# Kernel optimization log

Measured on AMD Instinct MI355X. Metric: run time of the kernel, lower is better.

Reference implementation:

```python
import jax, jax.numpy as jnp
import numpy as np

META_HIDDEN = 32


def _meta_apply(t, mw1, mb1, mw2, mb2):
    # t: [..., 3] triples; meta MLP 3 -> META_HIDDEN -> 1 (ReLU)
    h = jax.nn.relu(jnp.einsum('...k,hk->...h', t, mw1) + mb1)
    return jnp.einsum('...h,h->...', h, mw2[0]) + mb2[0]


def _meta_update_layer(v_in, w, v_out, mw1, mb1, mw2, mb2):
    # v_in: [I] (batch-0 input activations), w: [O, I], v_out: [O] (batch-0 output activations)
    # Builds the triples [v_i, w_ij, v_j] for every (i, j) pair and runs one batched meta pass.
    t = jnp.stack([
        jnp.broadcast_to(v_in[None, :], w.shape),
        w,
        jnp.broadcast_to(v_out[:, None], w.shape),
    ], axis=-1)  # [O, I, 3]
    return _meta_apply(t, mw1, mb1, mw2, mb2)  # [O, I] new weights


def setup_inputs() -> dict:
    key = jax.random.key(0)
    ks = jax.random.split(key, 12)
    I, H1, H2, O, B = 1024, 2048, 2048, 1024, 32
    def lin(kw, fan_in, fan_out):
        s = 1.0 / np.sqrt(fan_in)
        return jax.random.uniform(kw, (fan_out, fan_in), jnp.float32, -s, s)
    x = jax.random.normal(ks[0], (B, I), jnp.float32)
    w1 = lin(ks[1], I, H1); b1 = jax.random.uniform(ks[2], (H1,), jnp.float32, -1/np.sqrt(I), 1/np.sqrt(I))
    w2 = lin(ks[3], H1, H2); b2 = jax.random.uniform(ks[4], (H2,), jnp.float32, -1/np.sqrt(H1), 1/np.sqrt(H1))
    w3 = lin(ks[5], H2, O); b3 = jax.random.uniform(ks[6], (O,), jnp.float32, -1/np.sqrt(H2), 1/np.sqrt(H2))
    # meta network 3 -> META_HIDDEN -> 1
    mw1 = lin(ks[7], 3, META_HIDDEN); mb1 = jax.random.uniform(ks[8], (META_HIDDEN,), jnp.float32, -1/np.sqrt(3), 1/np.sqrt(3))
    mw2 = lin(ks[9], META_HIDDEN, 1); mb2 = jax.random.uniform(ks[10], (1,), jnp.float32, -1/np.sqrt(META_HIDDEN), 1/np.sqrt(META_HIDDEN))
    return {"x": x, "w1": w1, "b1": b1, "w2": w2, "b2": b2, "w3": w3, "b3": b3,
            "mw1": mw1, "mb1": mb1, "mw2": mw2, "mb2": mb2}


def reference(x, w1, b1, w2, b2, w3, b3, mw1, mb1, mw2, mb2):
    # Main 3-layer MLP forward (ReLU after every layer, including the last, as in the source).
    a0 = x
    a1 = jax.nn.relu(a0 @ w1.T + b1)
    a2 = jax.nn.relu(a1 @ w2.T + b2)
    out = jax.nn.relu(a2 @ w3.T + b3)
    # Per-weight meta update: original code loops over every (input, output) neuron pair of
    # each fc weight and writes meta_weight([v_i, w_ij, v_j]) back into the weight.
    # Only batch row 0 of the activations is used (impulse[i].data[0, idx]).
    nw1 = _meta_update_layer(a0[0], w1, a1[0], mw1, mb1, mw2, mb2)
    nw2 = _meta_update_layer(a1[0], w2, a2[0], mw1, mb1, mw2, mb2)
    nw3 = _meta_update_layer(a2[0], w3, out[0], mw1, mb1, mw2, mb2)
    return out, nw1, nw2, nw3
```

## Files before the change

kernel.cpp:

```cpp
#include <hip/hip_runtime.h>

#define NT 256

typedef unsigned int uint;
typedef unsigned short ushort_t;
typedef float f2 __attribute__((ext_vector_type(2)));
typedef short bh8 __attribute__((ext_vector_type(8)));
typedef float f32x4 __attribute__((ext_vector_type(4)));
typedef uint u32x4 __attribute__((ext_vector_type(4)));

__device__ __forceinline__ void gload16(const float* g, float* l) {
  __builtin_amdgcn_global_load_lds(
      (const __attribute__((address_space(1))) void*)g,
      (__attribute__((address_space(3))) void*)l, 16, 0, 0);
}

__device__ __forceinline__ uint hi2(float a, float b) {
  return (__float_as_uint(a) >> 16) | (__float_as_uint(b) & 0xffff0000u);
}
__device__ __forceinline__ uint lo2(float a, float b) {
  const float r0 = a - __uint_as_float(__float_as_uint(a) & 0xffff0000u);
  const float r1 = b - __uint_as_float(__float_as_uint(b) & 0xffff0000u);
  return hi2(r0, r1);
}
__device__ __forceinline__ void split8v(float4 v0, float4 v1, bh8& hi, bh8& lo) {
  u32x4 h = {hi2(v0.x, v0.y), hi2(v0.z, v0.w), hi2(v1.x, v1.y), hi2(v1.z, v1.w)};
  u32x4 t = {lo2(v0.x, v0.y), lo2(v0.z, v0.w), lo2(v1.x, v1.y), lo2(v1.z, v1.w)};
  hi = __builtin_bit_cast(bh8, h);
  lo = __builtin_bit_cast(bh8, t);
}

__device__ __forceinline__ void meta_body(
    int g,
    const float* __restrict__ w1, const float* __restrict__ w2, const float* __restrict__ w3,
    const float* __restrict__ a0, const float* __restrict__ r1, const float* __restrict__ r2,
    const float* __restrict__ bb1, const float* __restrict__ bb2, const float* __restrict__ bb3,
    float* __restrict__ n1, float* __restrict__ n2, float* __restrict__ n3,
    const float* __restrict__ mw1, const float* __restrict__ mb1,
    const float* __restrict__ mw2, const float* __restrict__ mb2) {
  const int n1c = (2048 * 1024) / 8;
  const int n2c = (2048 * 2048) / 8;

  const float* W; const float* vin; const float* bias; float* nw;
  int sh, e;
  if (g < n1c)            { W = w1; vin = a0; bias = bb1; nw = n1; sh = 10; e = g; }
  else if (g < n1c + n2c) { W = w2; vin = r1; bias = bb2; nw = n2; sh = 11; e = g - n1c; }
  else                    { W = w3; vin = r2; bias = bb3; nw = n3; sh = 11; e = g - n1c - n2c; }

  const int base = e << 3;
  const int o = base >> sh;
  const int i0 = base & ((1 << sh) - 1);
  const int tid = threadIdx.x;

  f2 wv[4], vv[4];
  {
    float4 t0 = *reinterpret_cast<const float4*>(&W[base]);
    float4 t1 = *reinterpret_cast<const float4*>(&W[base + 4]);
    wv[0] = (f2){t0.x, t0.y}; wv[1] = (f2){t0.z, t0.w};
    wv[2] = (f2){t1.x, t1.y}; wv[3] = (f2){t1.z, t1.w};
    float4 u0 = *reinterpret_cast<const float4*>(&vin[i0]);
    float4 u1 = *reinterpret_cast<const float4*>(&vin[i0 + 4]);
    vv[0] = (f2){u0.x, u0.y}; vv[1] = (f2){u0.z, u0.w};
    vv[2] = (f2){u1.x, u1.y}; vv[3] = (f2){u1.z, u1.w};
  }

  float part = 0.f;
  #pragma unroll
  for (int p = 0; p < 4; ++p)
    part += wv[p].x * vv[p].x + wv[p].y * vv[p].y;
  #pragma unroll
  for (int m = 32; m >= 1; m >>= 1)
    part += __shfl_xor(part, m, 64);
  __shared__ float msum[4];
  if ((tid & 63) == 0) msum[tid >> 6] = part;
  __syncthreads();
  float vo;
  if (sh == 10) vo = (tid < 128) ? (msum[0] + msum[1]) : (msum[2] + msum[3]);
  else          vo = (msum[0] + msum[1]) + (msum[2] + msum[3]);
  vo = fmaxf(vo + bias[o], 0.f);

  const float c2 = mb2[0];
  float r[32];
  #pragma unroll
  for (int j = 0; j < 32; ++j)
    r[j] = fmaf(mw1[3 * j + 2], vo, mb1[j]);

  f2 acc[4];
  #pragma unroll
  for (int p = 0; p < 4; ++p) acc[p] = (f2){c2, c2};

  const f2 zero = (f2){0.f, 0.f};
  #pragma unroll
  for (int j = 0; j < 32; ++j) {
    const float aj = mw1[3 * j];
    const float bj = mw1[3 * j + 1];
    const float mj = mw2[j];
    const f2 a2v = (f2){aj, aj};
    const f2 b2v = (f2){bj, bj};
    const f2 m2v = (f2){mj, mj};
    const f2 r2v = (f2){r[j], r[j]};
    #pragma unroll
    for (int p = 0; p < 4; ++p) {
#if __has_builtin(__builtin_elementwise_fma) && __has_builtin(__builtin_elementwise_max)
      f2 q = __builtin_elementwise_fma(a2v, vv[p], r2v);
      f2 h = __builtin_elementwise_fma(b2v, wv[p], q);
      h = __builtin_elementwise_max(h, zero);
      acc[p] = __builtin_elementwise_fma(m2v, h, acc[p]);
#else
      f2 h;
      h.x = fmaxf(fmaf(bj, wv[p].x, fmaf(aj, vv[p].x, r[j])), 0.f);
      h.y = fmaxf(fmaf(bj, wv[p].y, fmaf(aj, vv[p].y, r[j])), 0.f);
      acc[p].x = fmaf(mj, h.x, acc[p].x);
      acc[p].y = fmaf(mj, h.y, acc[p].y);
#endif
    }
  }

  *reinterpret_cast<float4*>(&nw[base])     = make_float4(acc[0].x, acc[0].y, acc[1].x, acc[1].y);
  *reinterpret_cast<float4*>(&nw[base + 4]) = make_float4(acc[2].x, acc[2].y, acc[3].x, acc[3].y);
}

template<int KL, int OBL, int AF32>
__device__ __forceinline__ void gemm_fwd(
    int gb, int tid,
    const float* __restrict__ Af32, const ushort_t* __restrict__ Ahi,
    const ushort_t* __restrict__ Alo,
    const float* __restrict__ W, int K, int O,
    float* __restrict__ P, float* __restrict__ Wt) {
  const int ob = gb & ((1 << OBL) - 1);
  const int sl = gb >> OBL;
  const int w = tid >> 6, l = tid & 63;
  const int l15 = l & 15, lk = l >> 4;
  const int b0 = (w & 1) << 4;
  const int ow = (w >> 1) << 6;
  const int obase = ob << 7;
  const int kbeg = sl * KL;
  const int bA = b0 + l15;

  f32x4 acc[4];
  #pragma unroll
  for (int of = 0; of < 4; ++of)
    #pragma unroll
    for (int e = 0; e < 4; ++e) acc[of][e] = 0.f;

  #pragma unroll 1
  for (int c = 0; c < KL / 32; ++c) {
    const int kc = kbeg + (c << 5);
    bh8 ahi, alo;
    const int kk = kc + (lk << 3);
    if constexpr (AF32) {
      const float4 v0 = *reinterpret_cast<const float4*>(&Af32[(size_t)bA * K + kk]);
      const float4 v1 = *reinterpret_cast<const float4*>(&Af32[(size_t)bA * K + kk + 4]);
      split8v(v0, v1, ahi, alo);
    } else {
      ahi = *reinterpret_cast<const bh8*>(&Ahi[(size_t)bA * K + kk]);
      alo = *reinterpret_cast<const bh8*>(&Alo[(size_t)bA * K + kk]);
    }
    #pragma unroll
    for (int q = 0; q < 4; ++q) {
      const int s = (q << 8) + tid;
      const int r = s >> 3;
      const int p = s & 7;
      const float* gp = &W[(size_t)(obase + r) * K + kc + ((p ^ (r & 7)) << 2)];
      gload16(gp, Wt + ((s & ~63) << 2));
    }
    __syncthreads();

    #pragma unroll
    for (int of = 0; of < 4; ++of) {
      const int lr = ow + (of << 4) + l15;
      const int cb = lk << 1;
      const float4 w0 = *reinterpret_cast<const float4*>(
          &Wt[(lr << 5) + ((cb ^ (lr & 7)) << 2)]);
      const float4 w1 = *reinterpret_cast<const float4*>(
          &Wt[(lr << 5) + (((cb + 1) ^ (lr & 7)) << 2)]);
      bh8 whi, wlo;
      split8v(w0, w1, whi, wlo);
      acc[of] = __builtin_amdgcn_mfma_f32_16x16x32_bf16(ahi, whi, acc[of], 0, 0, 0);
      acc[of] = __builtin_amdgcn_mfma_f32_16x16x32_bf16(ahi, wlo, acc[of], 0, 0, 0);
      acc[of] = __builtin_amdgcn_mfma_f32_16x16x32_bf16(alo, whi, acc[of], 0, 0, 0);
    }
    __syncthreads();
  }

  #pragma unroll
  for (int of = 0; of < 4; ++of) {
    const int o = obase + ow + (of << 4) + l15;
    #pragma unroll
    for (int r = 0; r < 4; ++r) {
      const int b = b0 + lk * 4 + r;
      P[((size_t)sl * 32 + b) * O + o] = acc[of][r];
    }
  }
}

template<int MODE, int OSH>
__device__ __forceinline__ void red_body(
    int lbid, int tid, const float* __restrict__ P, const float* __restrict__ bias,
    ushort_t* __restrict__ aHi, ushort_t* __restrict__ aLo,
    float* __restrict__ outF, float* __restrict__ row0) {
  const int idx = lbid * NT + tid;
  const int b = idx >> OSH;
  const int o = idx & ((1 << OSH) - 1);
  float s = 0.f;
  #pragma unroll
  for (int sl = 0; sl < 16; ++sl)
    s += P[(size_t)((sl * 32 + b) << OSH) + o];
  const float v = fmaxf(s + bias[o], 0.f);
  if constexpr (MODE == 0) {
    const uint u = __float_as_uint(v);
    aHi[(size_t)(b << OSH) + o] = (ushort_t)(u >> 16);
    const float hi = __uint_as_float(u & 0xffff0000u);
    aLo[(size_t)(b << OSH) + o] = (ushort_t)(__float_as_uint(v - hi) >> 16);
  } else {
    outF[(size_t)(b << OSH) + o] = v;
  }
  if (row0 != nullptr && b == 0) row0[o] = v;
}

template<int KL, int OBL, int AF32, int RMODE, int ROSH>
__global__ __launch_bounds__(NT) void fused(
    int nGemm, const float* Af32, const ushort_t* Ahi, const ushort_t* Alo,
    const float* W, int K, int O, float* P,
    int nRed, const float* RP, const float* Rb, ushort_t* rHi, ushort_t* rLo,
    float* rOut, float* rRow0,
    int mStart,
    const float* w1, const float* w2, const float* w3,
    const float* a0, const float* r1, const float* r2,
    const float* bb1, const float* bb2, const float* bb3,
    float* n1, float* n2, float* n3,
    const float* mw1, const float* mb1, const float* mw2, const float* mb2) {
  const int bid = blockIdx.x;
  const int tid = threadIdx.x;
  if (bid < nGemm) {
    __shared__ float Wt[128 * 32];
    gemm_fwd<KL, OBL, AF32>(bid, tid, Af32, Ahi, Alo, W, K, O, P, Wt);
    return;
  }
  int b = bid - nGemm;
  if (b < nRed) { red_body<RMODE, ROSH>(b, tid, RP, Rb, rHi, rLo, rOut, rRow0); return; }
  b -= nRed;
  const int g = mStart + b * NT + tid;
  meta_body(g, w1, w2, w3, a0, r1, r2, bb1, bb2, bb3,
            n1, n2, n3, mw1, mb1, mw2, mb2);
}

extern "C" void kernel_launch(void* const* d_in, const int* in_sizes, int n_in,
                              void* d_out, int out_size, void* d_ws, size_t ws_size,
                              hipStream_t stream) {
  const float* x   = (const float*)d_in[0];
  const float* w1  = (const float*)d_in[1];
  const float* b1  = (const float*)d_in[2];
  const float* w2  = (const float*)d_in[3];
  const float* b2  = (const float*)d_in[4];
  const float* w3  = (const float*)d_in[5];
  const float* b3  = (const float*)d_in[6];
  const float* mw1 = (const float*)d_in[7];
  const float* mb1 = (const float*)d_in[8];
  const float* mw2 = (const float*)d_in[9];
  const float* mb2 = (const float*)d_in[10];

  float* out = (float*)d_out;
  float* n1  = out + 32 * 1024;
  float* n2  = n1 + 2048 * 1024;
  float* n3  = n2 + 2048 * 2048;

  float* ws = (float*)d_ws;
  float* row01  = ws;
  float* row02  = row01 + 2048;
  ushort_t* a1hi = (ushort_t*)(row02 + 2048);
  ushort_t* a1lo = a1hi + 65536;
  ushort_t* a2hi = a1lo + 65536;
  ushort_t* a2lo = a2hi + 65536;
  float* P1 = (float*)(a2lo + 65536);
  float* P2 = P1 + 1048576;
  float* P3 = P2 + 1048576;


  #define MARGS w1, w2, w3, x, row01, row02, b1, b2, b3, n1, n2, n3, mw1, mb1, mw2, mb2
  #define NOGEMM 0, (const float*)nullptr, (const ushort_t*)nullptr, (const ushort_t*)nullptr, (const float*)nullptr, 0, 0, (float*)nullptr
  #define NORED  0, (const float*)nullptr, (const float*)nullptr, (ushort_t*)nullptr, (ushort_t*)nullptr, (float*)nullptr, (float*)nullptr

  fused<64, 4, 1, 0, 11><<<768, NT, 0, stream>>>(
      256, x, nullptr, nullptr, w1, 1024, 2048, P1,
      NORED, 0, MARGS);

  fused<64, 4, 0, 0, 11><<<768, NT, 0, stream>>>(
      NOGEMM,
      256, P1, b1, a1hi, a1lo, nullptr, row01,
      131072, MARGS);

  fused<128, 4, 0, 0, 11><<<1280, NT, 0, stream>>>(
      256, nullptr, a1hi, a1lo, w2, 2048, 2048, P2,
      NORED, 262144, MARGS);

  fused<64, 4, 0, 0, 11><<<1280, NT, 0, stream>>>(
      NOGEMM,
      256, P2, b2, a2hi, a2lo, nullptr, row02,
      524288, MARGS);

  fused<128, 3, 0, 0, 11><<<640, NT, 0, stream>>>(
      128, nullptr, a2hi, a2lo, w3, 2048, 1024, P3,
      NORED, 786432, MARGS);

  fused<64, 4, 0, 1, 10><<<640, NT, 0, stream>>>(
      NOGEMM,
      128, P3, b3, nullptr, nullptr, out, nullptr,
      917504, MARGS);

  #undef MARGS
  #undef NOGEMM
  #undef NORED
}
```

Before: 54.32 us.

## Fuse split-K reduction into GEMM blocks and cut launches from six to three

Each GEMM block now computes a 16-output tile over the full K, split across two wave pairs that combine partial sums through a small shared buffer, then applies bias, ReLU and the bf16 hi/lo split directly. This removes the separate reduction launches and the P partial-sum round trip through global memory. It also drops the LDS-staged weight tiles in favour of direct per-lane global loads, and the meta-update blocks are redistributed over the three remaining launches. The price is far fewer GEMM blocks (128/128/64) with long serial K loops, which may leave many CUs idle on the GEMM critical path.

```diff
diff --git a/kernel.cpp b/kernel.cpp
--- a/kernel.cpp
+++ b/kernel.cpp
@@ -8,12 +8,6 @@
 typedef short bh8 __attribute__((ext_vector_type(8)));
 typedef float f32x4 __attribute__((ext_vector_type(4)));
 typedef uint u32x4 __attribute__((ext_vector_type(4)));
-
-__device__ __forceinline__ void gload16(const float* g, float* l) {
-  __builtin_amdgcn_global_load_lds(
-      (const __attribute__((address_space(1))) void*)g,
-      (__attribute__((address_space(3))) void*)l, 16, 0, 0);
-}
 
 __device__ __forceinline__ uint hi2(float a, float b) {
   return (__float_as_uint(a) >> 16) | (__float_as_uint(b) & 0xffff0000u);
@@ -120,34 +114,29 @@
   *reinterpret_cast<float4*>(&nw[base + 4]) = make_float4(acc[2].x, acc[2].y, acc[3].x, acc[3].y);
 }
 
-template<int KL, int OBL, int AF32>
-__device__ __forceinline__ void gemm_fwd(
-    int gb, int tid,
-    const float* __restrict__ Af32, const ushort_t* __restrict__ Ahi,
-    const ushort_t* __restrict__ Alo,
-    const float* __restrict__ W, int K, int O,
-    float* __restrict__ P, float* __restrict__ Wt) {
-  const int ob = gb & ((1 << OBL) - 1);
-  const int sl = gb >> OBL;
+template<int AF32, int MODE>
+__device__ __forceinline__ void gemmF(
+    int ob, int tid, int K, int O,
+    const float* __restrict__ Af32,
+    const ushort_t* __restrict__ Ahi, const ushort_t* __restrict__ Alo,
+    const float* __restrict__ W, const float* __restrict__ bias,
+    ushort_t* __restrict__ aHi, ushort_t* __restrict__ aLo,
+    float* __restrict__ row0, float* __restrict__ outF,
+    float* __restrict__ comb ) {
   const int w = tid >> 6, l = tid & 63;
   const int l15 = l & 15, lk = l >> 4;
-  const int b0 = (w & 1) << 4;
-  const int ow = (w >> 1) << 6;
-  const int obase = ob << 7;
-  const int kbeg = sl * KL;
-  const int bA = b0 + l15;
-
-  f32x4 acc[4];
-  #pragma unroll
-  for (int of = 0; of < 4; ++of)
-    #pragma unroll
-    for (int e = 0; e < 4; ++e) acc[of][e] = 0.f;
-
-  #pragma unroll 1
-  for (int c = 0; c < KL / 32; ++c) {
-    const int kc = kbeg + (c << 5);
+  const int bh = w & 1, kh = w >> 1;
+  const int obase = ob << 4;
+  const int bA = (bh << 4) + l15;
+  const int kbeg = kh * (K >> 1);
+  const int kend = kbeg + (K >> 1);
+
+  f32x4 acc = {0.f, 0.f, 0.f, 0.f};
+
+  #pragma unroll 4
+  for (int k = kbeg; k < kend; k += 32) {
+    const int kk = k + (lk << 3);
     bh8 ahi, alo;
-    const int kk = kc + (lk << 3);
     if constexpr (AF32) {
       const float4 v0 = *reinterpret_cast<const float4*>(&Af32[(size_t)bA * K + kk]);
       const float4 v1 = *reinterpret_cast<const float4*>(&Af32[(size_t)bA * K + kk + 4]);
@@ -156,74 +145,47 @@
       ahi = *reinterpret_cast<const bh8*>(&Ahi[(size_t)bA * K + kk]);
       alo = *reinterpret_cast<const bh8*>(&Alo[(size_t)bA * K + kk]);
     }
-    #pragma unroll
-    for (int q = 0; q < 4; ++q) {
-      const int s = (q << 8) + tid;
-      const int r = s >> 3;
-      const int p = s & 7;
-      const float* gp = &W[(size_t)(obase + r) * K + kc + ((p ^ (r & 7)) << 2)];
-      gload16(gp, Wt + ((s & ~63) << 2));
-    }
-    __syncthreads();
-
-    #pragma unroll
-    for (int of = 0; of < 4; ++of) {
-      const int lr = ow + (of << 4) + l15;
-      const int cb = lk << 1;
-      const float4 w0 = *reinterpret_cast<const float4*>(
-          &Wt[(lr << 5) + ((cb ^ (lr & 7)) << 2)]);
-      const float4 w1 = *reinterpret_cast<const float4*>(
-          &Wt[(lr << 5) + (((cb + 1) ^ (lr & 7)) << 2)]);
-      bh8 whi, wlo;
-      split8v(w0, w1, whi, wlo);
-      acc[of] = __builtin_amdgcn_mfma_f32_16x16x32_bf16(ahi, whi, acc[of], 0, 0, 0);
-      acc[of] = __builtin_amdgcn_mfma_f32_16x16x32_bf16(ahi, wlo, acc[of], 0, 0, 0);
-      acc[of] = __builtin_amdgcn_mfma_f32_16x16x32_bf16(alo, whi, acc[of], 0, 0, 0);
-    }
-    __syncthreads();
-  }
-
-  #pragma unroll
-  for (int of = 0; of < 4; ++of) {
-    const int o = obase + ow + (of << 4) + l15;
+    const float4 w0 = *reinterpret_cast<const float4*>(&W[(size_t)(obase + l15) * K + kk]);
+    const float4 w1v = *reinterpret_cast<const float4*>(&W[(size_t)(obase + l15) * K + kk + 4]);
+    bh8 whi, wlo;
+    split8v(w0, w1v, whi, wlo);
+    acc = __builtin_amdgcn_mfma_f32_16x16x32_bf16(ahi, whi, acc, 0, 0, 0);
+    acc = __builtin_amdgcn_mfma_f32_16x16x32_bf16(ahi, wlo, acc, 0, 0, 0);
+    acc = __builtin_amdgcn_mfma_f32_16x16x32_bf16(alo, whi, acc, 0, 0, 0);
+  }
+
+  if (kh == 1) {
+    float* cw = comb + ((w * 64 + l) << 2);
+    cw[0] = acc[0]; cw[1] = acc[1]; cw[2] = acc[2]; cw[3] = acc[3];
+  }
+  __syncthreads();
+  if (kh == 0) {
+    const float* cp = comb + (((w + 2) * 64 + l) << 2);
     #pragma unroll
     for (int r = 0; r < 4; ++r) {
-      const int b = b0 + lk * 4 + r;
-      P[((size_t)sl * 32 + b) * O + o] = acc[of][r];
+      const int b = (bh << 4) + (lk << 2) + r;
+      const int o = obase + l15;
+      float v = acc[r] + cp[r];
+      v = fmaxf(v + bias[o], 0.f);
+      if constexpr (MODE == 0) {
+        const uint u = __float_as_uint(v);
+        aHi[(size_t)b * O + o] = (ushort_t)(u >> 16);
+        const float hi = __uint_as_float(u & 0xffff0000u);
+        aLo[(size_t)b * O + o] = (ushort_t)(__float_as_uint(v - hi) >> 16);
+        if (b == 0) row0[o] = v;
+      } else {
+        outF[(size_t)b * O + o] = v;
+      }
     }
   }
 }
 
-template<int MODE, int OSH>
-__device__ __forceinline__ void red_body(
-    int lbid, int tid, const float* __restrict__ P, const float* __restrict__ bias,
-    ushort_t* __restrict__ aHi, ushort_t* __restrict__ aLo,
-    float* __restrict__ outF, float* __restrict__ row0) {
-  const int idx = lbid * NT + tid;
-  const int b = idx >> OSH;
-  const int o = idx & ((1 << OSH) - 1);
-  float s = 0.f;
-  #pragma unroll
-  for (int sl = 0; sl < 16; ++sl)
-    s += P[(size_t)((sl * 32 + b) << OSH) + o];
-  const float v = fmaxf(s + bias[o], 0.f);
-  if constexpr (MODE == 0) {
-    const uint u = __float_as_uint(v);
-    aHi[(size_t)(b << OSH) + o] = (ushort_t)(u >> 16);
-    const float hi = __uint_as_float(u & 0xffff0000u);
-    aLo[(size_t)(b << OSH) + o] = (ushort_t)(__float_as_uint(v - hi) >> 16);
-  } else {
-    outF[(size_t)(b << OSH) + o] = v;
-  }
-  if (row0 != nullptr && b == 0) row0[o] = v;
-}
-
-template<int KL, int OBL, int AF32, int RMODE, int ROSH>
-__global__ __launch_bounds__(NT) void fused(
-    int nGemm, const float* Af32, const ushort_t* Ahi, const ushort_t* Alo,
-    const float* W, int K, int O, float* P,
-    int nRed, const float* RP, const float* Rb, ushort_t* rHi, ushort_t* rLo,
-    float* rOut, float* rRow0,
+template<int AF32, int MODE>
+__global__ __launch_bounds__(NT) void fusedF(
+    int nGemm, int K, int O,
+    const float* Af32, const ushort_t* Ahi, const ushort_t* Alo,
+    const float* W, const float* bias,
+    ushort_t* aHi, ushort_t* aLo, float* row0, float* outF,
     int mStart,
     const float* w1, const float* w2, const float* w3,
     const float* a0, const float* r1, const float* r2,
@@ -233,14 +195,12 @@
   const int bid = blockIdx.x;
   const int tid = threadIdx.x;
   if (bid < nGemm) {
-    __shared__ float Wt[128 * 32];
-    gemm_fwd<KL, OBL, AF32>(bid, tid, Af32, Ahi, Alo, W, K, O, P, Wt);
+    __shared__ float comb[4 * 64 * 4];
+    gemmF<AF32, MODE>(bid, tid, K, O, Af32, Ahi, Alo, W, bias,
+                      aHi, aLo, row0, outF, comb);
     return;
   }
-  int b = bid - nGemm;
-  if (b < nRed) { red_body<RMODE, ROSH>(b, tid, RP, Rb, rHi, rLo, rOut, rRow0); return; }
-  b -= nRed;
-  const int g = mStart + b * NT + tid;
+  const int g = (mStart + bid - nGemm) * NT + tid;
   meta_body(g, w1, w2, w3, a0, r1, r2, bb1, bb2, bb3,
             n1, n2, n3, mw1, mb1, mw2, mb2);
 }
@@ -272,43 +232,20 @@
   ushort_t* a1lo = a1hi + 65536;
   ushort_t* a2hi = a1lo + 65536;
   ushort_t* a2lo = a2hi + 65536;
-  float* P1 = (float*)(a2lo + 65536);
-  float* P2 = P1 + 1048576;
-  float* P3 = P2 + 1048576;
-
 
   #define MARGS w1, w2, w3, x, row01, row02, b1, b2, b3, n1, n2, n3, mw1, mb1, mw2, mb2
-  #define NOGEMM 0, (const float*)nullptr, (const ushort_t*)nullptr, (const ushort_t*)nullptr, (const float*)nullptr, 0, 0, (float*)nullptr
-  #define NORED  0, (const float*)nullptr, (const float*)nullptr, (ushort_t*)nullptr, (ushort_t*)nullptr, (float*)nullptr, (float*)nullptr
-
-  fused<64, 4, 1, 0, 11><<<768, NT, 0, stream>>>(
-      256, x, nullptr, nullptr, w1, 1024, 2048, P1,
-      NORED, 0, MARGS);
-
-  fused<64, 4, 0, 0, 11><<<768, NT, 0, stream>>>(
-      NOGEMM,
-      256, P1, b1, a1hi, a1lo, nullptr, row01,
-      131072, MARGS);
-
-  fused<128, 4, 0, 0, 11><<<1280, NT, 0, stream>>>(
-      256, nullptr, a1hi, a1lo, w2, 2048, 2048, P2,
-      NORED, 262144, MARGS);
-
-  fused<64, 4, 0, 0, 11><<<1280, NT, 0, stream>>>(
-      NOGEMM,
-      256, P2, b2, a2hi, a2lo, nullptr, row02,
-      524288, MARGS);
-
-  fused<128, 3, 0, 0, 11><<<640, NT, 0, stream>>>(
-      128, nullptr, a2hi, a2lo, w3, 2048, 1024, P3,
-      NORED, 786432, MARGS);
-
-  fused<64, 4, 0, 1, 10><<<640, NT, 0, stream>>>(
-      NOGEMM,
-      128, P3, b3, nullptr, nullptr, out, nullptr,
-      917504, MARGS);
+
+  fusedF<1, 0><<<128 + 1024, NT, 0, stream>>>(
+      128, 1024, 2048, x, nullptr, nullptr, w1, b1,
+      a1hi, a1lo, row01, nullptr, 0, MARGS);
+
+  fusedF<0, 0><<<128 + 2048, NT, 0, stream>>>(
+      128, 2048, 2048, nullptr, a1hi, a1lo, w2, b2,
+      a2hi, a2lo, row02, nullptr, 1024, MARGS);
+
+  fusedF<0, 1><<<64 + 1024, NT, 0, stream>>>(
+      64, 2048, 1024, nullptr, a2hi, a2lo, w3, b3,
+      nullptr, nullptr, nullptr, out, 3072, MARGS);
 
   #undef MARGS
-  #undef NOGEMM
-  #undef NORED
-}
+}
```

After: 60.43 us. 11.2% more time.
